# Optimization experiments

Measured on AMD Instinct MI355X. Metric: run time of the kernel, lower is better.

## Reference

```python
import jax, jax.numpy as jnp
import numpy as np

IN_DIM = 128
OUT_DIM = 128
NUM_HEADS = 4
HEAD_DIM = OUT_DIM // NUM_HEADS
TEMP = 0.2
NEG_SLOPE = 0.2


def _xavier(key, shape, gain=1.414):
    fan_in, fan_out = shape[-2], shape[-1]
    limit = gain * np.sqrt(6.0 / (fan_in + fan_out))
    return jax.random.uniform(key, shape, jnp.float32, -limit, limit)


def setup_inputs() -> dict:
    key = jax.random.key(0)
    k_h, k_W, k_a, k_mw, k_mb = jax.random.split(key, 5)
    B, N = 4, 2048
    h = jax.random.normal(k_h, (B, N, IN_DIM), jnp.float32)
    W = _xavier(k_W, (NUM_HEADS, IN_DIM, HEAD_DIM))
    a = _xavier(k_a, (NUM_HEADS, 2 * HEAD_DIM, 1))
    merge_w = _xavier(k_mw, (OUT_DIM, OUT_DIM))  # nn.Linear weight [out, in]
    merge_b = jnp.zeros((OUT_DIM,), jnp.float32)
    return {"h": h, "W": W, "a": a, "merge_w": merge_w, "merge_b": merge_b}


def reference(h, W, a, merge_w, merge_b):
    B, N, _ = h.shape
    # Wh: [B, H, N, head_dim]
    Wh = jnp.einsum('bni,hio->bhno', h, W)
    a_sq = a[..., 0]                                  # [H, 2*hd]
    a_src, a_dst = a_sq[:, :HEAD_DIM], a_sq[:, HEAD_DIM:]
    # additive score decomposition avoids the NxNx2hd concat blowup
    s_src = jnp.einsum('bhno,ho->bhn', Wh, a_src)     # contribution of node i (row)
    s_dst = jnp.einsum('bhno,ho->bhn', Wh, a_dst)     # contribution of node j (col)
    e = s_src[:, :, :, None] + s_dst[:, :, None, :]   # [B, H, N, N]
    e = jnp.where(e > 0, e, NEG_SLOPE * e)            # LeakyReLU(0.2)
    alpha = jax.nn.softmax(e / TEMP, axis=3)          # softmax over neighbors j
    h_prime_heads = jnp.einsum('bhnm,bhmo->bhno', alpha, Wh)
    h_concat = h_prime_heads.transpose(0, 2, 1, 3).reshape(B, N, OUT_DIM)
    h_prime = h_concat @ merge_w.T + merge_b
    return h_prime, alpha.mean(axis=1)
```

## Files before the change

### kernel.cpp

```cpp
#include <hip/hip_runtime.h>
#include <stddef.h>

#define NN 2048
#define DIN 128
#define HD 32

typedef __attribute__((ext_vector_type(8))) short short8;
typedef __attribute__((ext_vector_type(4))) float f32x4;

constexpr float SLOPE = 0.2f;
constexpr float LC = 7.2134752044448170f;

__device__ __forceinline__ unsigned int pack_rne(float a, float b){
    unsigned int xa = __float_as_uint(a), xb = __float_as_uint(b);
    unsigned int ra = (xa + 0x7fffu + ((xa >> 16) & 1u)) >> 16;
    unsigned int rb = (xb + 0x7fffu + ((xb >> 16) & 1u)) >> 16;
    return ra | (rb << 16);
}

__device__ __forceinline__ unsigned short bf16_rne(float a){
    unsigned int x = __float_as_uint(a);
    return (unsigned short)((x + 0x7fffu + ((x >> 16) & 1u)) >> 16);
}

__global__ __launch_bounds__(256) void kWh(const float* __restrict__ hg,
                                           const float* __restrict__ Wg,
                                           float* __restrict__ Wh)
{
    __shared__ float Wl[DIN*HD];
    __shared__ float Hl[8][DIN+4];
    const int t = threadIdx.x;
    const int bh = blockIdx.x >> 5;
    const int tile = blockIdx.x & 31;
    const int b = bh >> 2, hh = bh & 3;
    for (int i = t; i < DIN*HD; i += 256) Wl[i] = Wg[hh*DIN*HD + i];
    const int o = t & 31, r = t >> 5;
    for (int it = 0; it < 8; ++it){
        const int nb = tile*64 + it*8;
        __syncthreads();
        {
            const float4 v = *(const float4*)&hg[((size_t)b*NN + nb + r)*DIN + o*4];
            *(float4*)&Hl[r][o*4] = v;
        }
        __syncthreads();
        float acc = 0.f;
        #pragma unroll 8
        for (int i = 0; i < DIN; ++i) acc = fmaf(Hl[r][i], Wl[i*HD+o], acc);
        Wh[((size_t)bh*NN + nb + r)*HD + o] = acc;
    }
}

__global__ __launch_bounds__(256) void kScore(const float* __restrict__ Wh,
                                              const float* __restrict__ ag,
                                              float* __restrict__ sSrc,
                                              float* __restrict__ sDst,
                                              float* __restrict__ maxPart,
                                              unsigned short* __restrict__ WhT)
{
    __shared__ float al[64];
    __shared__ float wred[4];
    __shared__ unsigned short Tl[32][264];
    const int t = threadIdx.x;
    const int bh = blockIdx.x >> 3, seg = blockIdx.x & 7;
    const int hh = bh & 3;
    if (t < 64) al[t] = ag[hh*64 + t];
    __syncthreads();
    const int n = seg*256 + t;
    const float4* wr = (const float4*)&Wh[((size_t)bh*NN + n)*HD];
    float4 w[8];
    float ss = 0.f, sd = 0.f;
    #pragma unroll
    for (int q = 0; q < 8; ++q){
        w[q] = wr[q];
        ss += w[q].x*al[q*4+0] + w[q].y*al[q*4+1] + w[q].z*al[q*4+2] + w[q].w*al[q*4+3];
        sd += w[q].x*al[32+q*4+0] + w[q].y*al[32+q*4+1] + w[q].z*al[32+q*4+2] + w[q].w*al[32+q*4+3];
    }
    sSrc[bh*NN+n] = ss; sDst[bh*NN+n] = sd;
    #pragma unroll
    for (int q = 0; q < 8; ++q){
        const float* f = (const float*)&w[q];
        #pragma unroll
        for (int k2 = 0; k2 < 4; ++k2)
            Tl[q*4+k2][t] = bf16_rne(f[k2]);
    }
    float lmax = sd;
    #pragma unroll
    for (int off = 32; off > 0; off >>= 1) lmax = fmaxf(lmax, __shfl_down(lmax, off));
    if ((t & 63) == 0) wred[t >> 6] = lmax;
    __syncthreads();
    {
        const int o = t >> 3, ch = t & 7;
        const size_t base = ((size_t)bh*32 + o)*NN + seg*256;
        #pragma unroll
        for (int k = 0; k < 4; ++k)
            *(short8*)&WhT[base + k*64 + ch*8] = *(const short8*)&Tl[o][k*64 + ch*8];
    }
    if (t == 0) maxPart[bh*8 + seg] = fmaxf(fmaxf(wred[0], wred[1]), fmaxf(wred[2], wred[3]));
}

__global__ __launch_bounds__(256) void kAttnM(const unsigned short* __restrict__ WhT,
                                              const float* __restrict__ sSrc,
                                              const float* __restrict__ sDst,
                                              const float* __restrict__ maxPart,
                                              float* __restrict__ invZ,
                                              unsigned short* __restrict__ hcb)
{
    __shared__ float sdl[NN];
    const int t = threadIdx.x;
    const int lane = t & 63;
    const int wv = t >> 6;
    const int q = lane >> 4, c = lane & 15;
    const int bh = blockIdx.x >> 5;
    const int n0 = (blockIdx.x & 31)*64 + wv*16;
    const int b = bh >> 2, hh = bh & 3;
    for (int i = t; i < NN; i += 256) sdl[i] = LC * sDst[bh*NN + i];
    float mx = maxPart[bh*8];
    #pragma unroll
    for (int i = 1; i < 8; ++i) mx = fmaxf(mx, maxPart[bh*8 + i]);
    const float ssrc = sSrc[bh*NN + n0 + c];
    const float q0v = ssrc + mx;
    const float R = fmaxf(q0v, SLOPE*q0v) * LC;
    const float a1 = ssrc*LC - R;
    const float a2 = SLOPE*LC*ssrc - R;
    __syncthreads();
    const unsigned short* wb0 = WhT + (size_t)bh*32*NN + (size_t)c*NN + q*8;
    const unsigned short* wb1 = wb0 + (size_t)16*NN;
    f32x4 acc0 = {0.f,0.f,0.f,0.f}, acc1 = {0.f,0.f,0.f,0.f};
    float Zp = 0.f;
    short8 bF0 = *(const short8*)&wb0[0];
    short8 bF1 = *(const short8*)&wb1[0];
    #pragma unroll 4
    for (int it = 0; it < 64; ++it){
        const int m8 = it*32 + q*8;
        const int nx = ((it+1) & 63)*32;
        const short8 nF0 = *(const short8*)&wb0[nx];
        const short8 nF1 = *(const short8*)&wb1[nx];
        const f32x4 u0 = *(const f32x4*)&sdl[m8];
        const f32x4 u1 = *(const f32x4*)&sdl[m8+4];
        float p[8];
        #pragma unroll
        for (int j = 0; j < 4; ++j){
            p[j]   = exp2f(fmaxf(a1 + u0[j], fmaf(SLOPE, u0[j], a2)));
            p[4+j] = exp2f(fmaxf(a1 + u1[j], fmaf(SLOPE, u1[j], a2)));
        }
        short8 aF;
        #pragma unroll
        for (int j = 0; j < 8; j += 2){
            ((unsigned int*)&aF)[j>>1] = (__float_as_uint(p[j]) >> 16)
                                       | (__float_as_uint(p[j+1]) & 0xffff0000u);
            Zp += p[j] + p[j+1];
        }
        acc0 = __builtin_amdgcn_mfma_f32_16x16x32_bf16(aF, bF0, acc0, 0, 0, 0);
        acc1 = __builtin_amdgcn_mfma_f32_16x16x32_bf16(aF, bF1, acc1, 0, 0, 0);
        bF0 = nF0; bF1 = nF1;
    }
    Zp += __shfl_xor(Zp, 16);
    Zp += __shfl_xor(Zp, 32);
    const float iz = 1.0f / Zp;
    if (q == 0) invZ[bh*NN + n0 + c] = iz;
    #pragma unroll
    for (int reg = 0; reg < 4; ++reg){
        const int row = q*4 + reg;
        const float izr = __shfl(iz, row);
        const size_t base = ((size_t)b*NN + n0 + row)*128 + hh*32;
        hcb[base + c]      = (unsigned short)((pack_rne(acc0[reg]*izr, 0.f)) & 0xffffu);
        hcb[base + 16 + c] = (unsigned short)((pack_rne(acc1[reg]*izr, 0.f)) & 0xffffu);
    }
}

__global__ __launch_bounds__(256) void kAlpha(const float* __restrict__ sSrc,
                                              const float* __restrict__ sDst,
                                              const float* __restrict__ maxPart,
                                              const float* __restrict__ invZ,
                                              float* __restrict__ out1)
{
    __shared__ float sdl[4][NN];
    const int t = threadIdx.x;
    const int b = blockIdx.x >> 9;
    const int n0 = (blockIdx.x & 511) * 4;
    for (int i = t; i < 4*NN; i += 256)
        sdl[i >> 11][i & (NN-1)] = LC * sDst[(size_t)(b*4 + (i>>11))*NN + (i & (NN-1))];
    __syncthreads();
    float a1[4][4], a2[4][4], cf[4][4];
    #pragma unroll
    for (int hh = 0; hh < 4; ++hh){
        float mx = maxPart[(b*4+hh)*8];
        #pragma unroll
        for (int i = 1; i < 8; ++i) mx = fmaxf(mx, maxPart[(b*4+hh)*8 + i]);
        #pragma unroll
        for (int rr = 0; rr < 4; ++rr){
            const int bhn = (b*4+hh)*NN + n0 + rr;
            const float ss = sSrc[bhn];
            const float q0 = ss + mx;
            const float R = fmaxf(q0, SLOPE*q0)*LC;
            a1[rr][hh] = ss*LC - R;
            a2[rr][hh] = SLOPE*LC*ss - R;
            cf[rr][hh] = 0.25f * invZ[bhn];
        }
    }
    for (int mb = 0; mb < NN; mb += 256){
        const int m = mb + t;
        const float u0 = sdl[0][m], u1 = sdl[1][m], u2 = sdl[2][m], u3 = sdl[3][m];
        #pragma unroll
        for (int rr = 0; rr < 4; ++rr){
            float v;
            v  = cf[rr][0]*exp2f(fmaxf(a1[rr][0]+u0, fmaf(SLOPE, u0, a2[rr][0])));
            v += cf[rr][1]*exp2f(fmaxf(a1[rr][1]+u1, fmaf(SLOPE, u1, a2[rr][1])));
            v += cf[rr][2]*exp2f(fmaxf(a1[rr][2]+u2, fmaf(SLOPE, u2, a2[rr][2])));
            v += cf[rr][3]*exp2f(fmaxf(a1[rr][3]+u3, fmaf(SLOPE, u3, a2[rr][3])));
            out1[((size_t)b*NN + n0 + rr)*NN + m] = v;
        }
    }
}

__global__ __launch_bounds__(256) void kMergeM(const unsigned short* __restrict__ hcb,
                                               const float* __restrict__ mw,
                                               const float* __restrict__ mbv,
                                               float* __restrict__ out0)
{
    __shared__ unsigned short mwb[128][136];
    const int t = threadIdx.x;
    const int wv = t >> 6, lane = t & 63;
    const int q = lane >> 4, c = lane & 15;
    for (int i = t; i < 128*64; i += 256){
        const int j = i >> 6, k2 = i & 63;
        const float2 v = *(const float2*)&mw[j*128 + k2*2];
        *(unsigned int*)&mwb[j][k2*2] = pack_rne(v.x, v.y);
    }
    __syncthreads();
    const int row0 = blockIdx.x*64 + wv*16;
    f32x4 acc[8];
    #pragma unroll
    for (int ot = 0; ot < 8; ++ot) acc[ot] = (f32x4){0.f,0.f,0.f,0.f};
    #pragma unroll
    for (int ks = 0; ks < 4; ++ks){
        const short8 aF = *(const short8*)&hcb[((size_t)row0 + c)*128 + ks*32 + q*8];
        #pragma unroll
        for (int ot = 0; ot < 8; ++ot){
            const short8 bF = *(const short8*)&mwb[ot*16 + c][ks*32 + q*8];
            acc[ot] = __builtin_amdgcn_mfma_f32_16x16x32_bf16(aF, bF, acc[ot], 0, 0, 0);
        }
    }
    #pragma unroll
    for (int ot = 0; ot < 8; ++ot){
        const int col = ot*16 + c;
        const float bias = mbv[col];
        #pragma unroll
        for (int reg = 0; reg < 4; ++reg){
            const size_t row = (size_t)row0 + q*4 + reg;
            out0[row*128 + col] = acc[ot][reg] + bias;
        }
    }
}

extern "C" void kernel_launch(void* const* d_in, const int* in_sizes, int n_in,
                              void* d_out, int out_size, void* d_ws, size_t ws_size,
                              hipStream_t stream)
{
    const float* hg  = (const float*)d_in[0];
    const float* Wg  = (const float*)d_in[1];
    const float* ag  = (const float*)d_in[2];
    const float* mw  = (const float*)d_in[3];
    const float* mbv = (const float*)d_in[4];
    float* out0 = (float*)d_out;
    float* out1 = out0 + (size_t)4*NN*128;

    float* ws     = (float*)d_ws;
    float* Wh     = ws;
    float* sSrc   = Wh + 1048576;
    float* sDst   = sSrc + 32768;
    float* maxPart= sDst + 32768;
    float* invZ   = maxPart + 128;
    unsigned short* hcb = (unsigned short*)(invZ + 32768);
    unsigned short* WhT = hcb + 1048576;

    hipLaunchKernelGGL(kWh,    dim3(512),  dim3(256), 0, stream, hg, Wg, Wh);
    hipLaunchKernelGGL(kScore, dim3(128),  dim3(256), 0, stream, Wh, ag, sSrc, sDst, maxPart, WhT);
    hipLaunchKernelGGL(kAttnM, dim3(512),  dim3(256), 0, stream, WhT, sSrc, sDst, maxPart, invZ, hcb);
    hipLaunchKernelGGL(kAlpha, dim3(2048), dim3(256), 0, stream, sSrc, sDst, maxPart, invZ, out1);
    hipLaunchKernelGGL(kMergeM,dim3(128),  dim3(256), 0, stream, hcb, mw, mbv, out0);
}
```

Baseline: 165.8 us.

## Fuse projection and score kernels with split-bf16 MFMA, raw v_exp, prepacked weights

Replaces the scalar FP32 projection kernel and the separate score/transpose kernel with one kernel. It computes Wh via MFMA using a hi/lo bf16 split (three products) to keep near-FP32 accuracy, and writes the transposed bf16 WhT, source/destination scores and per-wave maxima directly. A small prep kernel converts W and the merge weight to bf16 once, so the merge kernel loses its per-block LDS conversion and runs on twice as many blocks. exp2f is replaced by the raw v_exp_f32 instruction in the attention and alpha kernels. This trades one extra launch and a less precise exponential for fewer global round trips of the FP32 Wh intermediate and less scalar ALU work.

```diff
diff --git a/kernel.cpp b/kernel.cpp
--- a/kernel.cpp
+++ b/kernel.cpp
@@ -7,6 +7,7 @@
 
 typedef __attribute__((ext_vector_type(8))) short short8;
 typedef __attribute__((ext_vector_type(4))) float f32x4;
+typedef __attribute__((ext_vector_type(4))) unsigned short us4;
 
 constexpr float SLOPE = 0.2f;
 constexpr float LC = 7.2134752044448170f;
@@ -23,89 +24,144 @@
     return (unsigned short)((x + 0x7fffu + ((x >> 16) & 1u)) >> 16);
 }
 
+__device__ __forceinline__ float fexp2(float x){
+    float r; asm("v_exp_f32 %0, %1" : "=v"(r) : "v"(x)); return r;
+}
+
+__global__ __launch_bounds__(256) void kPrep(const float* __restrict__ Wg,
+                                             const float* __restrict__ mw,
+                                             unsigned short* __restrict__ BtHi,
+                                             unsigned short* __restrict__ BtLo,
+                                             unsigned short* __restrict__ mwB)
+{
+    const int t = threadIdx.x;
+    if (blockIdx.x < 16){
+        const int col = blockIdx.x*8 + (t>>5);
+        const int i0  = (t&31)*4;
+        const int h = col >> 5, o = col & 31;
+        us4 vh, vl;
+        #pragma unroll
+        for (int j = 0; j < 4; ++j){
+            const float w = Wg[(h*DIN + i0 + j)*HD + o];
+            const unsigned short hi = bf16_rne(w);
+            const float hf = __uint_as_float((unsigned int)hi << 16);
+            vh[j] = hi;
+            vl[j] = bf16_rne(w - hf);
+        }
+        *(us4*)&BtHi[col*DIN + i0] = vh;
+        *(us4*)&BtLo[col*DIN + i0] = vl;
+    } else {
+        const int col = (blockIdx.x - 16)*8 + (t>>5);
+        const int k0  = (t&31)*4;
+        const f32x4 v = *(const f32x4*)&mw[col*128 + k0];
+        us4 p;
+        #pragma unroll
+        for (int j = 0; j < 4; ++j) p[j] = bf16_rne(v[j]);
+        *(us4*)&mwB[col*128 + k0] = p;
+    }
+}
+
 __global__ __launch_bounds__(256) void kWh(const float* __restrict__ hg,
-                                           const float* __restrict__ Wg,
-                                           float* __restrict__ Wh)
-{
-    __shared__ float Wl[DIN*HD];
-    __shared__ float Hl[8][DIN+4];
-    const int t = threadIdx.x;
-    const int bh = blockIdx.x >> 5;
-    const int tile = blockIdx.x & 31;
-    const int b = bh >> 2, hh = bh & 3;
-    for (int i = t; i < DIN*HD; i += 256) Wl[i] = Wg[hh*DIN*HD + i];
-    const int o = t & 31, r = t >> 5;
-    for (int it = 0; it < 8; ++it){
-        const int nb = tile*64 + it*8;
-        __syncthreads();
-        {
-            const float4 v = *(const float4*)&hg[((size_t)b*NN + nb + r)*DIN + o*4];
-            *(float4*)&Hl[r][o*4] = v;
-        }
-        __syncthreads();
-        float acc = 0.f;
-        #pragma unroll 8
-        for (int i = 0; i < DIN; ++i) acc = fmaf(Hl[r][i], Wl[i*HD+o], acc);
-        Wh[((size_t)bh*NN + nb + r)*HD + o] = acc;
-    }
-}
-
-__global__ __launch_bounds__(256) void kScore(const float* __restrict__ Wh,
-                                              const float* __restrict__ ag,
-                                              float* __restrict__ sSrc,
-                                              float* __restrict__ sDst,
-                                              float* __restrict__ maxPart,
-                                              unsigned short* __restrict__ WhT)
-{
-    __shared__ float al[64];
-    __shared__ float wred[4];
-    __shared__ unsigned short Tl[32][264];
-    const int t = threadIdx.x;
-    const int bh = blockIdx.x >> 3, seg = blockIdx.x & 7;
-    const int hh = bh & 3;
-    if (t < 64) al[t] = ag[hh*64 + t];
+                                           const unsigned short* __restrict__ BtHi,
+                                           const unsigned short* __restrict__ BtLo,
+                                           const float* __restrict__ ag,
+                                           unsigned short* __restrict__ WhT,
+                                           float* __restrict__ sSrc,
+                                           float* __restrict__ sDst,
+                                           float* __restrict__ maxPartW)
+{
+    __shared__ float Hl[16][DIN+4];
+    const int t = threadIdx.x;
+    const int wv = t >> 6, lane = t & 63;
+    const int q = lane >> 4, c = lane & 15;
+    const int r0 = blockIdx.x * 16;
+    const int b  = r0 >> 11;
+    const int n0 = r0 & (NN-1);
+    {
+        const int r = t >> 5, c4 = t & 31;
+        *(float4*)&Hl[r][c4*4] = *(const float4*)&hg[((size_t)b*NN + n0 + r)*DIN + c4*4];
+        const int f2 = t + 256, r2 = f2 >> 5, c42 = f2 & 31;
+        *(float4*)&Hl[r2][c42*4] = *(const float4*)&hg[((size_t)b*NN + n0 + r2)*DIN + c42*4];
+    }
     __syncthreads();
-    const int n = seg*256 + t;
-    const float4* wr = (const float4*)&Wh[((size_t)bh*NN + n)*HD];
-    float4 w[8];
-    float ss = 0.f, sd = 0.f;
-    #pragma unroll
-    for (int q = 0; q < 8; ++q){
-        w[q] = wr[q];
-        ss += w[q].x*al[q*4+0] + w[q].y*al[q*4+1] + w[q].z*al[q*4+2] + w[q].w*al[q*4+3];
-        sd += w[q].x*al[32+q*4+0] + w[q].y*al[32+q*4+1] + w[q].z*al[32+q*4+2] + w[q].w*al[32+q*4+3];
-    }
-    sSrc[bh*NN+n] = ss; sDst[bh*NN+n] = sd;
-    #pragma unroll
-    for (int q = 0; q < 8; ++q){
-        const float* f = (const float*)&w[q];
-        #pragma unroll
-        for (int k2 = 0; k2 < 4; ++k2)
-            Tl[q*4+k2][t] = bf16_rne(f[k2]);
-    }
-    float lmax = sd;
-    #pragma unroll
-    for (int off = 32; off > 0; off >>= 1) lmax = fmaxf(lmax, __shfl_down(lmax, off));
-    if ((t & 63) == 0) wred[t >> 6] = lmax;
-    __syncthreads();
+    short8 Ahi[4], Alo[4];
+    #pragma unroll
+    for (int k = 0; k < 4; ++k){
+        const float* sp = &Hl[c][k*32 + q*8];
+        #pragma unroll
+        for (int j2 = 0; j2 < 2; ++j2){
+            const f32x4 x = *(const f32x4*)&sp[j2*4];
+            #pragma unroll
+            for (int j = 0; j < 4; ++j){
+                const unsigned short hi = bf16_rne(x[j]);
+                const float hf = __uint_as_float((unsigned int)hi << 16);
+                ((unsigned short*)&Ahi[k])[j2*4+j] = hi;
+                ((unsigned short*)&Alo[k])[j2*4+j] = bf16_rne(x[j] - hf);
+            }
+        }
+    }
+    const int hh = wv;
+    const int bh = b*4 + hh;
+    f32x4 acc0 = {0.f,0.f,0.f,0.f}, acc1 = {0.f,0.f,0.f,0.f};
+    #pragma unroll
+    for (int k = 0; k < 4; ++k){
+        const int koff = k*32 + q*8;
+        const short8 Bh0 = *(const short8*)&BtHi[(hh*32      + c)*DIN + koff];
+        const short8 Bl0 = *(const short8*)&BtLo[(hh*32      + c)*DIN + koff];
+        const short8 Bh1 = *(const short8*)&BtHi[(hh*32 + 16 + c)*DIN + koff];
+        const short8 Bl1 = *(const short8*)&BtLo[(hh*32 + 16 + c)*DIN + koff];
+        acc0 = __builtin_amdgcn_mfma_f32_16x16x32_bf16(Ahi[k], Bh0, acc0, 0, 0, 0);
+        acc1 = __builtin_amdgcn_mfma_f32_16x16x32_bf16(Ahi[k], Bh1, acc1, 0, 0, 0);
+        acc0 = __builtin_amdgcn_mfma_f32_16x16x32_bf16(Ahi[k], Bl0, acc0, 0, 0, 0);
+        acc1 = __builtin_amdgcn_mfma_f32_16x16x32_bf16(Ahi[k], Bl1, acc1, 0, 0, 0);
+        acc0 = __builtin_amdgcn_mfma_f32_16x16x32_bf16(Alo[k], Bh0, acc0, 0, 0, 0);
+        acc1 = __builtin_amdgcn_mfma_f32_16x16x32_bf16(Alo[k], Bh1, acc1, 0, 0, 0);
+    }
     {
-        const int o = t >> 3, ch = t & 7;
-        const size_t base = ((size_t)bh*32 + o)*NN + seg*256;
-        #pragma unroll
-        for (int k = 0; k < 4; ++k)
-            *(short8*)&WhT[base + k*64 + ch*8] = *(const short8*)&Tl[o][k*64 + ch*8];
-    }
-    if (t == 0) maxPart[bh*8 + seg] = fmaxf(fmaxf(wred[0], wred[1]), fmaxf(wred[2], wred[3]));
+        us4 w0, w1;
+        #pragma unroll
+        for (int reg = 0; reg < 4; ++reg){
+            w0[reg] = bf16_rne(acc0[reg]);
+            w1[reg] = bf16_rne(acc1[reg]);
+        }
+        *(us4*)&WhT[((size_t)bh*32      + c)*NN + n0 + q*4] = w0;
+        *(us4*)&WhT[((size_t)bh*32 + 16 + c)*NN + n0 + q*4] = w1;
+    }
+    const float aS0 = ag[hh*64 + c],      aS1 = ag[hh*64 + 16 + c];
+    const float aD0 = ag[hh*64 + 32 + c], aD1 = ag[hh*64 + 48 + c];
+    float vs[4], vd[4];
+    #pragma unroll
+    for (int reg = 0; reg < 4; ++reg){
+        vs[reg] = acc0[reg]*aS0 + acc1[reg]*aS1;
+        vd[reg] = acc0[reg]*aD0 + acc1[reg]*aD1;
+    }
+    #pragma unroll
+    for (int m = 1; m <= 8; m <<= 1){
+        #pragma unroll
+        for (int reg = 0; reg < 4; ++reg){
+            vs[reg] += __shfl_xor(vs[reg], m);
+            vd[reg] += __shfl_xor(vd[reg], m);
+        }
+    }
+    if (c == 0){
+        *(f32x4*)&sSrc[(size_t)bh*NN + n0 + q*4] = (f32x4){vs[0],vs[1],vs[2],vs[3]};
+        *(f32x4*)&sDst[(size_t)bh*NN + n0 + q*4] = (f32x4){vd[0],vd[1],vd[2],vd[3]};
+    }
+    float wm = fmaxf(fmaxf(vd[0],vd[1]), fmaxf(vd[2],vd[3]));
+    wm = fmaxf(wm, __shfl_xor(wm, 16));
+    wm = fmaxf(wm, __shfl_xor(wm, 32));
+    if (lane == 0) maxPartW[bh*128 + (n0 >> 4)] = wm;
 }
 
 __global__ __launch_bounds__(256) void kAttnM(const unsigned short* __restrict__ WhT,
                                               const float* __restrict__ sSrc,
                                               const float* __restrict__ sDst,
-                                              const float* __restrict__ maxPart,
+                                              const float* __restrict__ maxPartW,
                                               float* __restrict__ invZ,
                                               unsigned short* __restrict__ hcb)
 {
     __shared__ float sdl[NN];
+    __shared__ float smax[4];
     const int t = threadIdx.x;
     const int lane = t & 63;
     const int wv = t >> 6;
@@ -114,15 +170,19 @@
     const int n0 = (blockIdx.x & 31)*64 + wv*16;
     const int b = bh >> 2, hh = bh & 3;
     for (int i = t; i < NN; i += 256) sdl[i] = LC * sDst[bh*NN + i];
-    float mx = maxPart[bh*8];
-    #pragma unroll
-    for (int i = 1; i < 8; ++i) mx = fmaxf(mx, maxPart[bh*8 + i]);
+    {
+        float v = maxPartW[bh*128 + ((wv&1)<<6) + lane];
+        #pragma unroll
+        for (int off = 32; off; off >>= 1) v = fmaxf(v, __shfl_xor(v, off));
+        if (lane == 0) smax[wv] = v;
+    }
     const float ssrc = sSrc[bh*NN + n0 + c];
+    __syncthreads();
+    const float mx = fmaxf(fmaxf(smax[0], smax[1]), fmaxf(smax[2], smax[3]));
     const float q0v = ssrc + mx;
     const float R = fmaxf(q0v, SLOPE*q0v) * LC;
     const float a1 = ssrc*LC - R;
     const float a2 = SLOPE*LC*ssrc - R;
-    __syncthreads();
     const unsigned short* wb0 = WhT + (size_t)bh*32*NN + (size_t)c*NN + q*8;
     const unsigned short* wb1 = wb0 + (size_t)16*NN;
     f32x4 acc0 = {0.f,0.f,0.f,0.f}, acc1 = {0.f,0.f,0.f,0.f};
@@ -140,8 +200,8 @@
         float p[8];
         #pragma unroll
         for (int j = 0; j < 4; ++j){
-            p[j]   = exp2f(fmaxf(a1 + u0[j], fmaf(SLOPE, u0[j], a2)));
-            p[4+j] = exp2f(fmaxf(a1 + u1[j], fmaf(SLOPE, u1[j], a2)));
+            p[j]   = fexp2(fmaxf(a1 + u0[j], fmaf(SLOPE, u0[j], a2)));
+            p[4+j] = fexp2(fmaxf(a1 + u1[j], fmaf(SLOPE, u1[j], a2)));
         }
         short8 aF;
         #pragma unroll
@@ -170,23 +230,29 @@
 
 __global__ __launch_bounds__(256) void kAlpha(const float* __restrict__ sSrc,
                                               const float* __restrict__ sDst,
-                                              const float* __restrict__ maxPart,
+                                              const float* __restrict__ maxPartW,
                                               const float* __restrict__ invZ,
                                               float* __restrict__ out1)
 {
     __shared__ float sdl[4][NN];
-    const int t = threadIdx.x;
+    __shared__ float mxl[4];
+    const int t = threadIdx.x;
+    const int wv = t >> 6, lane = t & 63;
     const int b = blockIdx.x >> 9;
     const int n0 = (blockIdx.x & 511) * 4;
+    {
+        float v = fmaxf(maxPartW[(b*4+wv)*128 + lane], maxPartW[(b*4+wv)*128 + 64 + lane]);
+        #pragma unroll
+        for (int off = 32; off; off >>= 1) v = fmaxf(v, __shfl_xor(v, off));
+        if (lane == 0) mxl[wv] = v;
+    }
     for (int i = t; i < 4*NN; i += 256)
         sdl[i >> 11][i & (NN-1)] = LC * sDst[(size_t)(b*4 + (i>>11))*NN + (i & (NN-1))];
     __syncthreads();
     float a1[4][4], a2[4][4], cf[4][4];
     #pragma unroll
     for (int hh = 0; hh < 4; ++hh){
-        float mx = maxPart[(b*4+hh)*8];
-        #pragma unroll
-        for (int i = 1; i < 8; ++i) mx = fmaxf(mx, maxPart[(b*4+hh)*8 + i]);
+        const float mx = mxl[hh];
         #pragma unroll
         for (int rr = 0; rr < 4; ++rr){
             const int bhn = (b*4+hh)*NN + n0 + rr;
@@ -204,50 +270,44 @@
         #pragma unroll
         for (int rr = 0; rr < 4; ++rr){
             float v;
-            v  = cf[rr][0]*exp2f(fmaxf(a1[rr][0]+u0, fmaf(SLOPE, u0, a2[rr][0])));
-            v += cf[rr][1]*exp2f(fmaxf(a1[rr][1]+u1, fmaf(SLOPE, u1, a2[rr][1])));
-            v += cf[rr][2]*exp2f(fmaxf(a1[rr][2]+u2, fmaf(SLOPE, u2, a2[rr][2])));
-            v += cf[rr][3]*exp2f(fmaxf(a1[rr][3]+u3, fmaf(SLOPE, u3, a2[rr][3])));
+            v  = cf[rr][0]*fexp2(fmaxf(a1[rr][0]+u0, fmaf(SLOPE, u0, a2[rr][0])));
+            v += cf[rr][1]*fexp2(fmaxf(a1[rr][1]+u1, fmaf(SLOPE, u1, a2[rr][1])));
+            v += cf[rr][2]*fexp2(fmaxf(a1[rr][2]+u2, fmaf(SLOPE, u2, a2[rr][2])));
+            v += cf[rr][3]*fexp2(fmaxf(a1[rr][3]+u3, fmaf(SLOPE, u3, a2[rr][3])));
             out1[((size_t)b*NN + n0 + rr)*NN + m] = v;
         }
     }
 }
 
 __global__ __launch_bounds__(256) void kMergeM(const unsigned short* __restrict__ hcb,
-                                               const float* __restrict__ mw,
+                                               const unsigned short* __restrict__ mwB,
                                                const float* __restrict__ mbv,
                                                float* __restrict__ out0)
 {
-    __shared__ unsigned short mwb[128][136];
     const int t = threadIdx.x;
     const int wv = t >> 6, lane = t & 63;
     const int q = lane >> 4, c = lane & 15;
-    for (int i = t; i < 128*64; i += 256){
-        const int j = i >> 6, k2 = i & 63;
-        const float2 v = *(const float2*)&mw[j*128 + k2*2];
-        *(unsigned int*)&mwb[j][k2*2] = pack_rne(v.x, v.y);
-    }
-    __syncthreads();
-    const int row0 = blockIdx.x*64 + wv*16;
-    f32x4 acc[8];
-    #pragma unroll
-    for (int ot = 0; ot < 8; ++ot) acc[ot] = (f32x4){0.f,0.f,0.f,0.f};
+    const int r0 = blockIdx.x*32 + (wv&1)*16;
+    const int ch = (wv>>1)*64;
+    f32x4 acc[4];
+    #pragma unroll
+    for (int ot = 0; ot < 4; ++ot) acc[ot] = (f32x4){0.f,0.f,0.f,0.f};
     #pragma unroll
     for (int ks = 0; ks < 4; ++ks){
-        const short8 aF = *(const short8*)&hcb[((size_t)row0 + c)*128 + ks*32 + q*8];
-        #pragma unroll
-        for (int ot = 0; ot < 8; ++ot){
-            const short8 bF = *(const short8*)&mwb[ot*16 + c][ks*32 + q*8];
+        const short8 aF = *(const short8*)&hcb[((size_t)r0 + c)*128 + ks*32 + q*8];
+        #pragma unroll
+        for (int ot = 0; ot < 4; ++ot){
+            const short8 bF = *(const short8*)&mwB[(size_t)(ch + ot*16 + c)*128 + ks*32 + q*8];
             acc[ot] = __builtin_amdgcn_mfma_f32_16x16x32_bf16(aF, bF, acc[ot], 0, 0, 0);
         }
     }
     #pragma unroll
-    for (int ot = 0; ot < 8; ++ot){
-        const int col = ot*16 + c;
+    for (int ot = 0; ot < 4; ++ot){
+        const int col = ch + ot*16 + c;
         const float bias = mbv[col];
         #pragma unroll
         for (int reg = 0; reg < 4; ++reg){
-            const size_t row = (size_t)row0 + q*4 + reg;
+            const size_t row = (size_t)r0 + q*4 + reg;
             out0[row*128 + col] = acc[ot][reg] + bias;
         }
     }
@@ -265,18 +325,20 @@
     float* out0 = (float*)d_out;
     float* out1 = out0 + (size_t)4*NN*128;
 
-    float* ws     = (float*)d_ws;
-    float* Wh     = ws;
-    float* sSrc   = Wh + 1048576;
-    float* sDst   = sSrc + 32768;
-    float* maxPart= sDst + 32768;
-    float* invZ   = maxPart + 128;
-    unsigned short* hcb = (unsigned short*)(invZ + 32768);
-    unsigned short* WhT = hcb + 1048576;
-
-    hipLaunchKernelGGL(kWh,    dim3(512),  dim3(256), 0, stream, hg, Wg, Wh);
-    hipLaunchKernelGGL(kScore, dim3(128),  dim3(256), 0, stream, Wh, ag, sSrc, sDst, maxPart, WhT);
-    hipLaunchKernelGGL(kAttnM, dim3(512),  dim3(256), 0, stream, WhT, sSrc, sDst, maxPart, invZ, hcb);
-    hipLaunchKernelGGL(kAlpha, dim3(2048), dim3(256), 0, stream, sSrc, sDst, maxPart, invZ, out1);
-    hipLaunchKernelGGL(kMergeM,dim3(128),  dim3(256), 0, stream, hcb, mw, mbv, out0);
-}
+    float* ws      = (float*)d_ws;
+    float* sSrc    = ws;
+    float* sDst    = sSrc + 32768;
+    float* maxPartW= sDst + 32768;
+    float* invZ    = maxPartW + 2048;
+    unsigned short* hcb  = (unsigned short*)(invZ + 32768);
+    unsigned short* WhT  = hcb + 1048576;
+    unsigned short* BtHi = WhT + 1048576;
+    unsigned short* BtLo = BtHi + 16384;
+    unsigned short* mwB  = BtLo + 16384;
+
+    hipLaunchKernelGGL(kPrep,  dim3(32),   dim3(256), 0, stream, Wg, mw, BtHi, BtLo, mwB);
+    hipLaunchKernelGGL(kWh,    dim3(512),  dim3(256), 0, stream, hg, BtHi, BtLo, ag, WhT, sSrc, sDst, maxPartW);
+    hipLaunchKernelGGL(kAttnM, dim3(512),  dim3(256), 0, stream, WhT, sSrc, sDst, maxPartW, invZ, hcb);
+    hipLaunchKernelGGL(kAlpha, dim3(2048), dim3(256), 0, stream, sSrc, sDst, maxPartW, invZ, out1);
+    hipLaunchKernelGGL(kMergeM,dim3(256),  dim3(256), 0, stream, hcb, mwB, mbv, out0);
+}
```

After: 143.2 us. 13.6% less time.
